# Kernel tuning notes

Measured on AMD Instinct MI355X. Metric: run time of the kernel, lower is better.

## Reference

```python
import jax, jax.numpy as jnp
import numpy as np

D_MODEL = 1024
N_HEADS = 16
HEAD_DIM = D_MODEL // N_HEADS


def setup_inputs() -> dict:
    key = jax.random.key(0)
    k1, k2, k3 = jax.random.split(key, 3)
    scale = 0.02
    x = jax.random.normal(k1, (2, 2048, D_MODEL), dtype=jnp.float32)
    w_qkv = jax.random.normal(k2, (D_MODEL, 3 * D_MODEL), dtype=jnp.float32) * scale
    b_qkv = jnp.zeros((3 * D_MODEL,), dtype=jnp.float32)
    w_proj = jax.random.normal(k3, (D_MODEL, D_MODEL), dtype=jnp.float32) * scale
    b_proj = jnp.zeros((D_MODEL,), dtype=jnp.float32)
    return {"x": x, "w_qkv": w_qkv, "b_qkv": b_qkv, "w_proj": w_proj, "b_proj": b_proj}


def reference(x, w_qkv, b_qkv, w_proj, b_proj):
    bsz, seq_len, d_model = x.shape
    qkv = x @ w_qkv + b_qkv  # [B,S,3D]
    q, k, v = jnp.split(qkv, 3, axis=-1)
    # [B,S,D] -> [B,H,S,hd]
    def to_heads(t):
        return t.reshape(bsz, seq_len, N_HEADS, HEAD_DIM).transpose(0, 2, 1, 3)
    q, k, v = to_heads(q), to_heads(k), to_heads(v)
    scores = jnp.einsum("bhqd,bhkd->bhqk", q, k) / jnp.sqrt(jnp.float32(HEAD_DIM))
    causal = jnp.triu(jnp.ones((seq_len, seq_len), dtype=bool), k=1)
    scores = jnp.where(causal, -jnp.inf, scores)
    attn = jax.nn.softmax(scores, axis=-1)
    out = jnp.einsum("bhqk,bhkd->bhqd", attn, v)  # [B,H,S,hd]
    out = out.transpose(0, 2, 1, 3).reshape(bsz, seq_len, d_model)
    return out @ w_proj + b_proj
```

## Files before the change

kernel.cpp:

```cpp
#include <hip/hip_runtime.h>
#include <hip/hip_bf16.h>

#define D_MODEL 1024
#define SEQ     2048
#define NH      16
#define HD      64
#define M_TOK   4096
#define THREE_D 3072

using bf16x8 = __bf16 __attribute__((ext_vector_type(8)));
using bf16x4 = __bf16 __attribute__((ext_vector_type(4)));
using f32x4  = float  __attribute__((ext_vector_type(4)));

typedef __attribute__((address_space(3))) uint32_t lds_u32;
typedef const __attribute__((address_space(1))) uint32_t glb_u32;

__global__ __launch_bounds__(256) void cast_kernel(const float* __restrict__ in,
                                                   __bf16* __restrict__ out, int n4) {
  int i = blockIdx.x * 256 + threadIdx.x;
  if (i < n4) {
    float4 f = reinterpret_cast<const float4*>(in)[i];
    bf16x4 o;
    o[0] = (__bf16)f.x; o[1] = (__bf16)f.y; o[2] = (__bf16)f.z; o[3] = (__bf16)f.w;
    reinterpret_cast<bf16x4*>(out)[i] = o;
  }
}

__global__ __launch_bounds__(256) void transpose_cast(const float* __restrict__ in,
                                                      __bf16* __restrict__ out, int R, int C) {
  __shared__ float tile[64][65];
  int c0 = blockIdx.x * 64, r0 = blockIdx.y * 64;
  int tx = threadIdx.x & 63, ty = threadIdx.x >> 6;
#pragma unroll
  for (int i = 0; i < 16; ++i) {
    int r = ty + i * 4;
    tile[r][tx] = in[(size_t)(r0 + r) * C + c0 + tx];
  }
  __syncthreads();
#pragma unroll
  for (int i = 0; i < 16; ++i) {
    int r = ty + i * 4;
    out[(size_t)(c0 + r) * R + r0 + tx] = (__bf16)tile[tx][r];
  }
}

__global__ __launch_bounds__(256, 3) void gemm_qkv(const __bf16* __restrict__ A,
                                                   const __bf16* __restrict__ BT,
                                                   const float* __restrict__ bias,
                                                   __bf16* __restrict__ qb, __bf16* __restrict__ kb,
                                                   __bf16* __restrict__ vb) {
  __shared__ __bf16 As[3][128 * 32];
  __shared__ __bf16 Bs[3][128 * 32];
  const int Kdim = D_MODEL;
  const int tid  = threadIdx.x;
  const int lane = tid & 63, wave = tid >> 6;
  const int lr = lane & 15, lg = lane >> 4;
  const int wm = (wave >> 1) * 64, wn = (wave & 1) * 64;
  const int m0 = blockIdx.y * 128, n0 = blockIdx.x * 128;
  const int srow = tid >> 2, scol = (tid & 3) * 8;

  f32x4 acc[4][4] = {};

  const __bf16* aSrc = A  + (size_t)(m0 + srow) * Kdim + scol;
  const __bf16* bSrc = BT + (size_t)(n0 + srow) * Kdim + scol;

  auto stage = [&](int p, int k0) {
    __builtin_amdgcn_global_load_lds((glb_u32*)(aSrc + k0),              (lds_u32*)(As[p] + wave * 512),        16, 0, 0);
    __builtin_amdgcn_global_load_lds((glb_u32*)(aSrc + 64 * Kdim + k0), (lds_u32*)(As[p] + wave * 512 + 2048), 16, 0, 0);
    __builtin_amdgcn_global_load_lds((glb_u32*)(bSrc + k0),              (lds_u32*)(Bs[p] + wave * 512),        16, 0, 0);
    __builtin_amdgcn_global_load_lds((glb_u32*)(bSrc + 64 * Kdim + k0), (lds_u32*)(Bs[p] + wave * 512 + 2048), 16, 0, 0);
  };

  const int nk = Kdim / 32;
  stage(0, 0);
  stage(1, 32);
  for (int kk = 0; kk < nk; ++kk) {
    const int cur = kk % 3;
    if (kk + 2 < nk) {
      stage((kk + 2) % 3, (kk + 2) * 32);
      asm volatile("s_waitcnt vmcnt(8)" ::: "memory");
    } else if (kk + 1 < nk) {
      asm volatile("s_waitcnt vmcnt(4)" ::: "memory");
    } else {
      asm volatile("s_waitcnt vmcnt(0)" ::: "memory");
    }
    __builtin_amdgcn_s_barrier();

    bf16x8 af[4], bfv[4];
#pragma unroll
    for (int i = 0; i < 4; ++i) af[i]  = *reinterpret_cast<const bf16x8*>(&As[cur][(wm + i * 16 + lr) * 32 + lg * 8]);
#pragma unroll
    for (int j = 0; j < 4; ++j) bfv[j] = *reinterpret_cast<const bf16x8*>(&Bs[cur][(wn + j * 16 + lr) * 32 + lg * 8]);
#pragma unroll
    for (int i = 0; i < 4; ++i)
#pragma unroll
      for (int j = 0; j < 4; ++j)
        acc[i][j] = __builtin_amdgcn_mfma_f32_16x16x32_bf16(af[i], bfv[j], acc[i][j], 0, 0, 0);

    asm volatile("s_waitcnt lgkmcnt(0)" ::: "memory");
    __builtin_amdgcn_s_barrier();
  }

#pragma unroll
  for (int i = 0; i < 4; ++i) {
#pragma unroll
    for (int j = 0; j < 4; ++j) {
      const int gc = n0 + wn + j * 16 + lr;
      const float bv = bias[gc];
      const int t = gc >> 10, rem = gc & 1023;
      const int h = rem >> 6, d = rem & 63;
#pragma unroll
      for (int ii = 0; ii < 4; ++ii) {
        const int gr = m0 + wm + i * 16 + lg * 4 + ii;
        const float val = acc[i][j][ii] + bv;
        const int b = gr >> 11, s = gr & 2047;
        if (t == 0) {
          qb[(((size_t)(b * NH + h)) * SEQ + s) * HD + d] = (__bf16)(val * 0.125f);
        } else if (t == 1) {
          kb[(((size_t)(b * NH + h)) * SEQ + s) * HD + d] = (__bf16)val;
        } else {
          vb[(((size_t)(b * NH + h)) * HD + d) * SEQ + s] = (__bf16)val;
        }
      }
    }
  }
}

__global__ __launch_bounds__(256, 4) void gemm_proj(const __bf16* __restrict__ A,
                                                    const __bf16* __restrict__ BT,
                                                    const float* __restrict__ bias,
                                                    float* __restrict__ fout) {
  __shared__ __bf16 As[3][64 * 32];
  __shared__ __bf16 Bs[3][128 * 32];
  const int Kdim = D_MODEL;
  const int tid  = threadIdx.x;
  const int lane = tid & 63, wave = tid >> 6;
  const int lr = lane & 15, lg = lane >> 4;
  const int wm = (wave >> 1) * 32, wn = (wave & 1) * 64;
  const int n0 = blockIdx.x * 128, m0 = blockIdx.y * 64;
  const int srow = tid >> 2, scol = (tid & 3) * 8;

  f32x4 acc[2][4] = {};

  const __bf16* aSrc = A  + (size_t)(m0 + srow) * Kdim + scol;
  const __bf16* bSrc = BT + (size_t)(n0 + srow) * Kdim + scol;

  auto stage = [&](int p, int k0) {
    __builtin_amdgcn_global_load_lds((glb_u32*)(aSrc + k0),              (lds_u32*)(As[p] + wave * 512),        16, 0, 0);
    __builtin_amdgcn_global_load_lds((glb_u32*)(bSrc + k0),              (lds_u32*)(Bs[p] + wave * 512),        16, 0, 0);
    __builtin_amdgcn_global_load_lds((glb_u32*)(bSrc + 64 * Kdim + k0), (lds_u32*)(Bs[p] + wave * 512 + 2048), 16, 0, 0);
  };

  const int nk = Kdim / 32;
  stage(0, 0);
  stage(1, 32);
  for (int kk = 0; kk < nk; ++kk) {
    const int cur = kk % 3;
    if (kk + 2 < nk) {
      stage((kk + 2) % 3, (kk + 2) * 32);
      asm volatile("s_waitcnt vmcnt(6)" ::: "memory");
    } else if (kk + 1 < nk) {
      asm volatile("s_waitcnt vmcnt(3)" ::: "memory");
    } else {
      asm volatile("s_waitcnt vmcnt(0)" ::: "memory");
    }
    __builtin_amdgcn_s_barrier();

    bf16x8 af[2], bfv[4];
#pragma unroll
    for (int i = 0; i < 2; ++i) af[i]  = *reinterpret_cast<const bf16x8*>(&As[cur][(wm + i * 16 + lr) * 32 + lg * 8]);
#pragma unroll
    for (int j = 0; j < 4; ++j) bfv[j] = *reinterpret_cast<const bf16x8*>(&Bs[cur][(wn + j * 16 + lr) * 32 + lg * 8]);
#pragma unroll
    for (int i = 0; i < 2; ++i)
#pragma unroll
      for (int j = 0; j < 4; ++j)
        acc[i][j] = __builtin_amdgcn_mfma_f32_16x16x32_bf16(af[i], bfv[j], acc[i][j], 0, 0, 0);

    asm volatile("s_waitcnt lgkmcnt(0)" ::: "memory");
    __builtin_amdgcn_s_barrier();
  }

#pragma unroll
  for (int i = 0; i < 2; ++i) {
#pragma unroll
    for (int j = 0; j < 4; ++j) {
      const int gc = n0 + wn + j * 16 + lr;
      const float bv = bias[gc];
#pragma unroll
      for (int ii = 0; ii < 4; ++ii) {
        const int gr = m0 + wm + i * 16 + lg * 4 + ii;
        fout[(size_t)gr * D_MODEL + gc] = acc[i][j][ii] + bv;
      }
    }
  }
}

__global__ __launch_bounds__(256, 4) void attn_kernel(const __bf16* __restrict__ Q,
                                                      const __bf16* __restrict__ K,
                                                      const __bf16* __restrict__ VT,
                                                      __bf16* __restrict__ AO) {
  __shared__ __bf16 Kb[2][64 * 64];
  __shared__ __bf16 Vb[2][64 * 64];
  __shared__ __bf16 Ps[4][16 * 64];

  const int tid  = threadIdx.x;
  const int lane = tid & 63, wave = tid >> 6;
  const int lr = lane & 15, lg = lane >> 4;

  const int f  = blockIdx.x;
  const int c  = f & 7;
  const int u  = f >> 3;
  const int bh = c * 4 + (u & 3);
  const int s2 = u >> 2, grp = s2 >> 3, r = s2 & 7;
  const int qblk = (grp == 0) ? (31 - r) : (grp == 1) ? r : (grp == 2) ? (39 - s2) : (s2 - 16);

  const int q0 = qblk * 64 + wave * 16;
  const size_t base = (size_t)bh * SEQ * HD;
  const char* Kg  = (const char*)(K + base);
  const char* VTg = (const char*)(VT + base);

  bf16x8 qf[2];
#pragma unroll
  for (int kc = 0; kc < 2; ++kc)
    qf[kc] = *reinterpret_cast<const bf16x8*>(Q + base + (size_t)(q0 + lr) * HD + kc * 32 + lg * 8);

  float lrun[4] = {0.f, 0.f, 0.f, 0.f};
  f32x4 o[4] = {};

  const int nt = qblk + 1;
  const int nmaxF = (wave | 1) + 1;

  auto stage = [&](int bufp, int t) {
    const int k0 = t * 64;
#pragma unroll
    for (int p = 0; p < 2; ++p) {
      const int row = wave * 16 + p * 8 + (lane >> 3);
      {
        const int srcOff = (k0 + row) * 128 + (((lane & 7) ^ (row & 7)) << 4);
        __builtin_amdgcn_global_load_lds((glb_u32*)(Kg + srcOff),
                                         (lds_u32*)&Kb[bufp][(wave * 16 + p * 8) * 64], 16, 0, 0);
      }
      {
        const int srcOff = row * 4096 + k0 * 2 + (((lane & 7) ^ (row & 7)) << 4);
        __builtin_amdgcn_global_load_lds((glb_u32*)(VTg + srcOff),
                                         (lds_u32*)&Vb[bufp][(wave * 16 + p * 8) * 64], 16, 0, 0);
      }
    }
  };

  stage(0, 0);
  asm volatile("s_waitcnt vmcnt(0)" ::: "memory");
  __syncthreads();

  for (int t = 0; t < nt; ++t) {
    const int p = t & 1;
    const int k0 = t * 64;
    const bool last = (t == nt - 1);
    const int nmax = last ? nmaxF : 4;
    const int kcmax = nmax >> 1;

    if (t + 1 < nt) stage(p ^ 1, t + 1);

    const __bf16* Kt = Kb[p];
    const __bf16* Vt = Vb[p];

    f32x4 s[4] = {};
#pragma unroll
    for (int kc = 0; kc < 2; ++kc) {
#pragma unroll
      for (int n = 0; n < 4; ++n)
        if (n < nmax) {
          bf16x8 kf = *reinterpret_cast<const bf16x8*>(
              &Kt[(n * 16 + lr) * 64 + (((kc * 4 + lg) ^ (lr & 7)) << 3)]);
          s[n] = __builtin_amdgcn_mfma_f32_16x16x32_bf16(qf[kc], kf, s[n], 0, 0, 0);
        }
    }

    if (last) {
#pragma unroll
      for (int n = 0; n < 4; ++n)
        if (n < nmax)
#pragma unroll
          for (int ii = 0; ii < 4; ++ii) {
            int qg = q0 + lg * 4 + ii;
            int kg = k0 + n * 16 + lr;
            if (kg > qg) s[n][ii] = -__builtin_inff();
          }
    }

#pragma unroll
    for (int n = 0; n < 4; ++n)
      if (n < nmax)
#pragma unroll
        for (int ii = 0; ii < 4; ++ii) {
          float pv = __expf(s[n][ii]);
          lrun[ii] += pv;
          const int row = lg * 4 + ii;
          Ps[wave][row * 64 + (((n * 2 + (lr >> 3)) ^ (row & 7)) << 3) + (lr & 7)] = (__bf16)pv;
        }

#pragma unroll
    for (int kc = 0; kc < 2; ++kc)
      if (kc < kcmax) {
        bf16x8 pa = *reinterpret_cast<const bf16x8*>(
            &Ps[wave][lr * 64 + (((kc * 4 + lg) ^ (lr & 7)) << 3)]);
#pragma unroll
        for (int nd = 0; nd < 4; ++nd) {
          bf16x8 vf = *reinterpret_cast<const bf16x8*>(
              &Vt[(nd * 16 + lr) * 64 + (((kc * 4 + lg) ^ (lr & 7)) << 3)]);
          o[nd] = __builtin_amdgcn_mfma_f32_16x16x32_bf16(pa, vf, o[nd], 0, 0, 0);
        }
      }

    asm volatile("s_waitcnt vmcnt(0)" ::: "memory");
    __syncthreads();
  }

#pragma unroll
  for (int off = 1; off <= 8; off <<= 1)
#pragma unroll
    for (int ii = 0; ii < 4; ++ii) lrun[ii] += __shfl_xor(lrun[ii], off, 64);

  const int b = bh >> 4, h = bh & 15;
  float rl[4];
#pragma unroll
  for (int ii = 0; ii < 4; ++ii) rl[ii] = 1.f / lrun[ii];
#pragma unroll
  for (int nd = 0; nd < 4; ++nd)
#pragma unroll
    for (int ii = 0; ii < 4; ++ii) {
      int row = q0 + lg * 4 + ii;
      AO[((size_t)(b * SEQ) + row) * D_MODEL + h * HD + nd * 16 + lr] = (__bf16)(o[nd][ii] * rl[ii]);
    }
}

extern "C" void kernel_launch(void* const* d_in, const int* in_sizes, int n_in,
                              void* d_out, int out_size, void* d_ws, size_t ws_size,
                              hipStream_t stream) {
  const float* x      = (const float*)d_in[0];
  const float* w_qkv  = (const float*)d_in[1];
  const float* b_qkv  = (const float*)d_in[2];
  const float* w_proj = (const float*)d_in[3];
  const float* b_proj = (const float*)d_in[4];
  float* out = (float*)d_out;

  char* ws = (char*)d_ws;
  __bf16* xb     = (__bf16*)(ws);
  __bf16* wqkvT  = (__bf16*)(ws + 8388608);
  __bf16* wprojT = (__bf16*)(ws + 14680064);
  __bf16* qb     = (__bf16*)(ws + 16777216);
  __bf16* kb     = (__bf16*)(ws + 25165824);
  __bf16* vtb    = (__bf16*)(ws + 33554432);
  __bf16* ao     = (__bf16*)(ws + 41943040);

  cast_kernel<<<4096, 256, 0, stream>>>(x, xb, M_TOK * D_MODEL / 4);
  transpose_cast<<<dim3(THREE_D / 64, D_MODEL / 64), 256, 0, stream>>>(w_qkv, wqkvT, D_MODEL, THREE_D);
  transpose_cast<<<dim3(D_MODEL / 64, D_MODEL / 64), 256, 0, stream>>>(w_proj, wprojT, D_MODEL, D_MODEL);

  gemm_qkv<<<dim3(THREE_D / 128, M_TOK / 128), 256, 0, stream>>>(
      xb, wqkvT, b_qkv, qb, kb, vtb);

  attn_kernel<<<1024, 256, 0, stream>>>(qb, kb, vtb, ao);

  gemm_proj<<<dim3(D_MODEL / 128, M_TOK / 64), 256, 0, stream>>>(
      ao, wprojT, b_proj, out);
}
```

Baseline: 114.6 us.

## Widen attention blocks to 128 queries, swizzle QKV GEMM tiles, vectorize V stores

The attention kernel now runs 512 threads (8 waves) per block covering 128 query rows. Each staged K/V tile is shared by twice as many queries, which halves redundant K/V loads, and the diagonal masking is split across two tile steps. The QKV GEMM uses a 1D grid with a swizzle that groups blocks by row for better cache locality, and it writes the transposed V output as 4-wide bf16 vectors. The larger blocks may lower occupancy, and waves in the first half sit idle on the final tile.

```diff
diff --git a/kernel.cpp b/kernel.cpp
--- a/kernel.cpp
+++ b/kernel.cpp
@@ -56,7 +56,11 @@
   const int lane = tid & 63, wave = tid >> 6;
   const int lr = lane & 15, lg = lane >> 4;
   const int wm = (wave >> 1) * 64, wn = (wave & 1) * 64;
-  const int m0 = blockIdx.y * 128, n0 = blockIdx.x * 128;
+
+  const int f   = blockIdx.x;
+  const int swz = (f & 7) * 96 + (f >> 3);
+  const int m0  = (swz / 24) * 128, n0 = (swz % 24) * 128;
+
   const int srow = tid >> 2, scol = (tid & 3) * 8;
 
   f32x4 acc[4][4] = {};
@@ -101,25 +105,38 @@
     __builtin_amdgcn_s_barrier();
   }
 
-#pragma unroll
-  for (int i = 0; i < 4; ++i) {
+  const int reg = n0 >> 10;
+  if (reg == 2) {
 #pragma unroll
     for (int j = 0; j < 4; ++j) {
       const int gc = n0 + wn + j * 16 + lr;
       const float bv = bias[gc];
-      const int t = gc >> 10, rem = gc & 1023;
-      const int h = rem >> 6, d = rem & 63;
-#pragma unroll
-      for (int ii = 0; ii < 4; ++ii) {
-        const int gr = m0 + wm + i * 16 + lg * 4 + ii;
-        const float val = acc[i][j][ii] + bv;
-        const int b = gr >> 11, s = gr & 2047;
-        if (t == 0) {
-          qb[(((size_t)(b * NH + h)) * SEQ + s) * HD + d] = (__bf16)(val * 0.125f);
-        } else if (t == 1) {
-          kb[(((size_t)(b * NH + h)) * SEQ + s) * HD + d] = (__bf16)val;
-        } else {
-          vb[(((size_t)(b * NH + h)) * HD + d) * SEQ + s] = (__bf16)val;
+      const int rem = gc & 1023, h = rem >> 6, d = rem & 63;
+#pragma unroll
+      for (int i = 0; i < 4; ++i) {
+        const int gr0 = m0 + wm + i * 16 + lg * 4;
+        const int b = gr0 >> 11, s0 = gr0 & 2047;
+        bf16x4 v4;
+#pragma unroll
+        for (int ii = 0; ii < 4; ++ii) v4[ii] = (__bf16)(acc[i][j][ii] + bv);
+        *reinterpret_cast<bf16x4*>(&vb[(((size_t)(b * NH + h)) * HD + d) * SEQ + s0]) = v4;
+      }
+    }
+  } else {
+#pragma unroll
+    for (int i = 0; i < 4; ++i) {
+#pragma unroll
+      for (int j = 0; j < 4; ++j) {
+        const int gc = n0 + wn + j * 16 + lr;
+        const float bv = bias[gc];
+        const int rem = gc & 1023, h = rem >> 6, d = rem & 63;
+#pragma unroll
+        for (int ii = 0; ii < 4; ++ii) {
+          const int gr = m0 + wm + i * 16 + lg * 4 + ii;
+          const float val = acc[i][j][ii] + bv;
+          const int b = gr >> 11, s = gr & 2047;
+          if (reg == 0) qb[(((size_t)(b * NH + h)) * SEQ + s) * HD + d] = (__bf16)(val * 0.125f);
+          else          kb[(((size_t)(b * NH + h)) * SEQ + s) * HD + d] = (__bf16)val;
         }
       }
     }
@@ -196,13 +213,13 @@
   }
 }
 
-__global__ __launch_bounds__(256, 4) void attn_kernel(const __bf16* __restrict__ Q,
+__global__ __launch_bounds__(512, 4) void attn_kernel(const __bf16* __restrict__ Q,
                                                       const __bf16* __restrict__ K,
                                                       const __bf16* __restrict__ VT,
                                                       __bf16* __restrict__ AO) {
   __shared__ __bf16 Kb[2][64 * 64];
   __shared__ __bf16 Vb[2][64 * 64];
-  __shared__ __bf16 Ps[4][16 * 64];
+  __shared__ __bf16 Ps[8][16 * 64];
 
   const int tid  = threadIdx.x;
   const int lane = tid & 63, wave = tid >> 6;
@@ -212,10 +229,10 @@
   const int c  = f & 7;
   const int u  = f >> 3;
   const int bh = c * 4 + (u & 3);
-  const int s2 = u >> 2, grp = s2 >> 3, r = s2 & 7;
-  const int qblk = (grp == 0) ? (31 - r) : (grp == 1) ? r : (grp == 2) ? (39 - s2) : (s2 - 16);
-
-  const int q0 = qblk * 64 + wave * 16;
+  const int s2 = u >> 2;
+  const int qblk = (s2 < 8) ? (15 - s2) : (s2 - 8);
+
+  const int q0 = qblk * 128 + wave * 16;
   const size_t base = (size_t)bh * SEQ * HD;
   const char* Kg  = (const char*)(K + base);
   const char* VTg = (const char*)(VT + base);
@@ -228,24 +245,21 @@
   float lrun[4] = {0.f, 0.f, 0.f, 0.f};
   f32x4 o[4] = {};
 
-  const int nt = qblk + 1;
-  const int nmaxF = (wave | 1) + 1;
+  const int nt = 2 * qblk + 2;
+  const int nmaxD = ((wave & 3) | 1) + 1;
 
   auto stage = [&](int bufp, int t) {
     const int k0 = t * 64;
-#pragma unroll
-    for (int p = 0; p < 2; ++p) {
-      const int row = wave * 16 + p * 8 + (lane >> 3);
-      {
-        const int srcOff = (k0 + row) * 128 + (((lane & 7) ^ (row & 7)) << 4);
-        __builtin_amdgcn_global_load_lds((glb_u32*)(Kg + srcOff),
-                                         (lds_u32*)&Kb[bufp][(wave * 16 + p * 8) * 64], 16, 0, 0);
-      }
-      {
-        const int srcOff = row * 4096 + k0 * 2 + (((lane & 7) ^ (row & 7)) << 4);
-        __builtin_amdgcn_global_load_lds((glb_u32*)(VTg + srcOff),
-                                         (lds_u32*)&Vb[bufp][(wave * 16 + p * 8) * 64], 16, 0, 0);
-      }
+    const int row = wave * 8 + (lane >> 3);
+    {
+      const int srcOff = (k0 + row) * 128 + (((lane & 7) ^ (row & 7)) << 4);
+      __builtin_amdgcn_global_load_lds((glb_u32*)(Kg + srcOff),
+                                       (lds_u32*)&Kb[bufp][(wave * 8) * 64], 16, 0, 0);
+    }
+    {
+      const int srcOff = row * 4096 + k0 * 2 + (((lane & 7) ^ (row & 7)) << 4);
+      __builtin_amdgcn_global_load_lds((glb_u32*)(VTg + srcOff),
+                                       (lds_u32*)&Vb[bufp][(wave * 8) * 64], 16, 0, 0);
     }
   };
 
@@ -256,8 +270,14 @@
   for (int t = 0; t < nt; ++t) {
     const int p = t & 1;
     const int k0 = t * 64;
-    const bool last = (t == nt - 1);
-    const int nmax = last ? nmaxF : 4;
+    int nmax = 4;
+    bool diag = false;
+    if (wave < 4) {
+      if (t == nt - 2) { nmax = nmaxD; diag = true; }
+      else if (t == nt - 1) nmax = 0;
+    } else {
+      if (t == nt - 1) { nmax = nmaxD; diag = true; }
+    }
     const int kcmax = nmax >> 1;
 
     if (t + 1 < nt) stage(p ^ 1, t + 1);
@@ -265,53 +285,55 @@
     const __bf16* Kt = Kb[p];
     const __bf16* Vt = Vb[p];
 
-    f32x4 s[4] = {};
-#pragma unroll
-    for (int kc = 0; kc < 2; ++kc) {
-#pragma unroll
-      for (int n = 0; n < 4; ++n)
-        if (n < nmax) {
-          bf16x8 kf = *reinterpret_cast<const bf16x8*>(
-              &Kt[(n * 16 + lr) * 64 + (((kc * 4 + lg) ^ (lr & 7)) << 3)]);
-          s[n] = __builtin_amdgcn_mfma_f32_16x16x32_bf16(qf[kc], kf, s[n], 0, 0, 0);
-        }
-    }
-
-    if (last) {
+    if (nmax > 0) {
+      f32x4 s[4] = {};
+#pragma unroll
+      for (int kc = 0; kc < 2; ++kc) {
+#pragma unroll
+        for (int n = 0; n < 4; ++n)
+          if (n < nmax) {
+            bf16x8 kf = *reinterpret_cast<const bf16x8*>(
+                &Kt[(n * 16 + lr) * 64 + (((kc * 4 + lg) ^ (lr & 7)) << 3)]);
+            s[n] = __builtin_amdgcn_mfma_f32_16x16x32_bf16(qf[kc], kf, s[n], 0, 0, 0);
+          }
+      }
+
+      if (diag) {
+#pragma unroll
+        for (int n = 0; n < 4; ++n)
+          if (n < nmax)
+#pragma unroll
+            for (int ii = 0; ii < 4; ++ii) {
+              int qg = q0 + lg * 4 + ii;
+              int kg = k0 + n * 16 + lr;
+              if (kg > qg) s[n][ii] = -__builtin_inff();
+            }
+      }
+
 #pragma unroll
       for (int n = 0; n < 4; ++n)
         if (n < nmax)
 #pragma unroll
           for (int ii = 0; ii < 4; ++ii) {
-            int qg = q0 + lg * 4 + ii;
-            int kg = k0 + n * 16 + lr;
-            if (kg > qg) s[n][ii] = -__builtin_inff();
+            float pv = __expf(s[n][ii]);
+            lrun[ii] += pv;
+            const int row = lg * 4 + ii;
+            Ps[wave][row * 64 + (((n * 2 + (lr >> 3)) ^ (row & 7)) << 3) + (lr & 7)] = (__bf16)pv;
           }
-    }
-
-#pragma unroll
-    for (int n = 0; n < 4; ++n)
-      if (n < nmax)
-#pragma unroll
-        for (int ii = 0; ii < 4; ++ii) {
-          float pv = __expf(s[n][ii]);
-          lrun[ii] += pv;
-          const int row = lg * 4 + ii;
-          Ps[wave][row * 64 + (((n * 2 + (lr >> 3)) ^ (row & 7)) << 3) + (lr & 7)] = (__bf16)pv;
+
+#pragma unroll
+      for (int kc = 0; kc < 2; ++kc)
+        if (kc < kcmax) {
+          bf16x8 pa = *reinterpret_cast<const bf16x8*>(
+              &Ps[wave][lr * 64 + (((kc * 4 + lg) ^ (lr & 7)) << 3)]);
+#pragma unroll
+          for (int nd = 0; nd < 4; ++nd) {
+            bf16x8 vf = *reinterpret_cast<const bf16x8*>(
+                &Vt[(nd * 16 + lr) * 64 + (((kc * 4 + lg) ^ (lr & 7)) << 3)]);
+            o[nd] = __builtin_amdgcn_mfma_f32_16x16x32_bf16(pa, vf, o[nd], 0, 0, 0);
+          }
         }
-
-#pragma unroll
-    for (int kc = 0; kc < 2; ++kc)
-      if (kc < kcmax) {
-        bf16x8 pa = *reinterpret_cast<const bf16x8*>(
-            &Ps[wave][lr * 64 + (((kc * 4 + lg) ^ (lr & 7)) << 3)]);
-#pragma unroll
-        for (int nd = 0; nd < 4; ++nd) {
-          bf16x8 vf = *reinterpret_cast<const bf16x8*>(
-              &Vt[(nd * 16 + lr) * 64 + (((kc * 4 + lg) ^ (lr & 7)) << 3)]);
-          o[nd] = __builtin_amdgcn_mfma_f32_16x16x32_bf16(pa, vf, o[nd], 0, 0, 0);
-        }
-      }
+    }
 
     asm volatile("s_waitcnt vmcnt(0)" ::: "memory");
     __syncthreads();
@@ -358,10 +380,9 @@
   transpose_cast<<<dim3(THREE_D / 64, D_MODEL / 64), 256, 0, stream>>>(w_qkv, wqkvT, D_MODEL, THREE_D);
   transpose_cast<<<dim3(D_MODEL / 64, D_MODEL / 64), 256, 0, stream>>>(w_proj, wprojT, D_MODEL, D_MODEL);
 
-  gemm_qkv<<<dim3(THREE_D / 128, M_TOK / 128), 256, 0, stream>>>(
-      xb, wqkvT, b_qkv, qb, kb, vtb);
-
-  attn_kernel<<<1024, 256, 0, stream>>>(qb, kb, vtb, ao);
+  gemm_qkv<<<768, 256, 0, stream>>>(xb, wqkvT, b_qkv, qb, kb, vtb);
+
+  attn_kernel<<<512, 512, 0, stream>>>(qb, kb, vtb, ao);
 
   gemm_proj<<<dim3(D_MODEL / 128, M_TOK / 64), 256, 0, stream>>>(
       ao, wprojT, b_proj, out);
```

After: 117.3 us. +2.4%, slower.
